# Performance work log

Measured on AMD Instinct MI355X. Metric: run time of the kernel, lower is better.

The kernel has to match this reference:

```python
import jax, jax.numpy as jnp
import numpy as np

B, S, H, F_IN = 256, 128, 512, 1


def _lstm_step(h, c, x, Wih, Whh, b):
    # PyTorch LSTM gate order: i, f, g, o
    gates = x @ Wih.T + h @ Whh.T + b  # (B, 4H)
    i, f, g, o = jnp.split(gates, 4, axis=-1)
    c = jax.nn.sigmoid(f) * c + jax.nn.sigmoid(i) * jnp.tanh(g)
    h = jax.nn.sigmoid(o) * jnp.tanh(c)
    return h, c


def setup_inputs() -> dict:
    key = jax.random.key(0)
    ks = jax.random.split(key, 18)
    p = lambda k, shape: (jax.random.normal(k, shape, dtype=jnp.float32) * 0.05)
    return {
        "input_seq": jax.random.normal(ks[0], (B, S, F_IN), dtype=jnp.float32),
        # encoder: embedding Linear(F_IN -> H) + LSTM(H -> H)
        "We_e": p(ks[1], (H, F_IN)), "be_e": p(ks[2], (H,)),
        "Wih_e": p(ks[3], (4 * H, H)), "Whh_e": p(ks[4], (4 * H, H)), "b_e": p(ks[5], (4 * H,)),
        # decoder: embedding Linear(F_IN -> H) + LSTMCell(H -> H)
        "We_d": p(ks[6], (H, F_IN)), "be_d": p(ks[7], (H,)),
        "Wih_d": p(ks[8], (4 * H, H)), "Whh_d": p(ks[9], (4 * H, H)), "b_d": p(ks[10], (4 * H,)),
        # additive attention: W_1, W_2 (H->H), v (H->1)
        "W1": p(ks[11], (H, H)), "b1": p(ks[12], (H,)),
        "W2": p(ks[13], (H, H)), "b2": p(ks[14], (H,)),
        "v": p(ks[15], (1, H)), "bv": p(ks[16], (1,)),
    }


def reference(input_seq, We_e, be_e, Wih_e, Whh_e, b_e,
              We_d, be_d, Wih_d, Whh_d, b_d,
              W1, b1, W2, b2, v, bv):
    # ---- encoder: embed then LSTM over the sequence ----
    emb = input_seq @ We_e.T + be_e  # (B, S, H)

    def enc_step(carry, x_t):
        h, c = carry
        h, c = _lstm_step(h, c, x_t, Wih_e, Whh_e, b_e)
        return (h, c), h

    h0 = jnp.zeros((B, H), dtype=input_seq.dtype)
    (h, c), enc_h = jax.lax.scan(enc_step, (h0, h0), jnp.swapaxes(emb, 0, 1))
    encoder_output = jnp.swapaxes(enc_h, 0, 1)  # (B, S, H)

    # W_1(encoder_output) is loop-invariant; hoist it (same math as the
    # original, which redundantly recomputes it every step).
    w1enc = encoder_output @ W1.T + b1  # (B, S, H)

    # ---- decoder: per-step LSTMCell + additive attention ----
    def dec_step(carry, _):
        hd, cd, x_in = carry
        e = x_in @ We_d.T + be_d  # (B, H)
        hd, cd = _lstm_step(hd, cd, e, Wih_d, Whh_d, b_d)
        q = hd @ W2.T + b2  # (B, H)
        u = jnp.squeeze(jnp.tanh(w1enc + q[:, None, :]) @ v.T + bv, -1)  # (B, S)
        att = jax.nn.log_softmax(u, axis=1)
        idx = jnp.argmax(att, axis=1)  # pointer (B,)
        # next decoder input = pointed-to input symbol
        x_next = jnp.take_along_axis(input_seq[:, :, 0], idx[:, None], axis=1)  # (B, 1)
        return (hd, cd, x_next), (att, idx)

    x0 = jnp.zeros((B, 1), dtype=input_seq.dtype)
    _, (scores, ptrs) = jax.lax.scan(dec_step, (h, c, x0), None, length=S)
    pointers_scores = jnp.swapaxes(scores, 0, 1)  # (B, S, S) log-probs
    pointers = jnp.swapaxes(ptrs, 0, 1)  # (B, S) int
    return pointers_scores, pointers
```

## Files before the change

kernel.cpp:

```cpp
#include <hip/hip_runtime.h>
#include <hip/hip_fp16.h>

#define Bn 256
#define Sn 128
#define Hn 512
#define G4 2048
#define NBLK 256
#define NTHR 1024
#define HSTR 516

typedef float f4v __attribute__((ext_vector_type(4)));
typedef unsigned u4v __attribute__((ext_vector_type(4)));

__device__ __forceinline__ float sigf(float x){
    float e = expf(-fabsf(x));
    float d = 1.f + e;
    return x >= 0.f ? 1.f/d : e/d;
}

__device__ __forceinline__ float cload(const float* p){
    return __hip_atomic_load((float*)p, __ATOMIC_RELAXED, __HIP_MEMORY_SCOPE_AGENT);
}
__device__ __forceinline__ void cstore(float* p, float v){
    __hip_atomic_store(p, v, __ATOMIC_RELAXED, __HIP_MEMORY_SCOPE_AGENT);
}

__device__ __forceinline__ void gbar(unsigned* cnt, unsigned k){
    __syncthreads();
    if (threadIdx.x == 0) {
        __hip_atomic_fetch_add(cnt, 1u, __ATOMIC_RELAXED, __HIP_MEMORY_SCOPE_AGENT);
        while (__hip_atomic_load(cnt, __ATOMIC_RELAXED, __HIP_MEMORY_SCOPE_AGENT) < 16u*k)
            __builtin_amdgcn_s_sleep(1);
        asm volatile("" ::: "memory");
    }
    __syncthreads();
}
__device__ __forceinline__ void gbar_sys(unsigned* cnt, unsigned k){
    __syncthreads();
    if (threadIdx.x == 0) {
        __hip_atomic_fetch_add(cnt, 1u, __ATOMIC_RELEASE, __HIP_MEMORY_SCOPE_AGENT);
        while (__hip_atomic_load(cnt, __ATOMIC_RELAXED, __HIP_MEMORY_SCOPE_AGENT) < 16u*k)
            __builtin_amdgcn_s_sleep(1);
        (void)__hip_atomic_load(cnt, __ATOMIC_ACQUIRE, __HIP_MEMORY_SCOPE_AGENT);
    }
    __syncthreads();
}

__global__ void precompute_kernel(
    const float* __restrict__ Wih_e, const float* __restrict__ We_e,
    const float* __restrict__ be_e,  const float* __restrict__ b_e,
    const float* __restrict__ Wih_d, const float* __restrict__ We_d,
    const float* __restrict__ be_d,  const float* __restrict__ b_d,
    float* __restrict__ p1, float* __restrict__ p0,
    float* __restrict__ r1, float* __restrict__ r0)
{
    int j = blockIdx.x*blockDim.x + threadIdx.x;
    bool dec = j >= G4;
    int jj = dec ? j - G4 : j;
    const float* Wih = dec ? Wih_d : Wih_e;
    const float* We  = dec ? We_d  : We_e;
    const float* be  = dec ? be_d  : be_e;
    const float* bb  = dec ? b_d   : b_e;
    float s1 = 0.f, s0 = 0.f;
    for (int k = 0; k < Hn; ++k) {
        float w = Wih[jj*Hn + k];
        s1 += w * We[k];
        s0 += w * be[k];
    }
    s0 += bb[jj];
    if (dec) { r1[jj] = s1; r0[jj] = s0; }
    else     { p1[jj] = s1; p0[jj] = s0; }
}

template<bool WEF>
__global__ __launch_bounds__(NTHR, 4) void ptrnet_kernel(
    const float* __restrict__ xseq,
    const float* __restrict__ Whh_e, const float* __restrict__ Whh_d,
    const float* __restrict__ W1, const float* __restrict__ b1,
    const float* __restrict__ W2, const float* __restrict__ b2,
    const float* __restrict__ vv,
    const float* __restrict__ p1, const float* __restrict__ p0,
    const float* __restrict__ r1, const float* __restrict__ r0,
    float* __restrict__ hb0, float* __restrict__ hb1,
    float* __restrict__ cbuf, float* __restrict__ qbuf,
    float* __restrict__ x_in, void* __restrict__ w1enc,
    unsigned* __restrict__ barb,
    float* __restrict__ out_scores, float* __restrict__ out_ptr)
{
    __shared__ float smem[16*HSTR + 512*5 + 16];
    float* hs  = smem;
    float* red = smem + 16*HSTR;
    float* qs  = smem;
    float* vs  = smem + Hn;
    float* us  = smem + 2*Hn;
    float* rr  = smem + 2*Hn + Sn + 8;

    const int blk = blockIdx.x;
    const int tid = threadIdx.x;
    const int bt  = blk >> 4, grp = blk & 15;
    const int b0  = bt << 4;
    const int tb  = tid & 15;
    const int hh  = (tid >> 4) & 31;
    const int ks  = tid >> 9;
    const int hg  = (grp << 5) + hh;
    const int kofs = ks << 8;
    unsigned* gcnt = barb + bt*64;
    unsigned bk = 0;
    float* hprev = hb0;
    float* hnext = hb1;

#define STAGE_H(SRC) do { \
    for (int i_ = tid; i_ < 16*Hn; i_ += NTHR) { \
        int r_ = i_ >> 9, k_ = i_ & (Hn-1); \
        hs[r_*HSTR + k_] = cload((SRC) + (size_t)(b0+r_)*Hn + k_); \
    } __syncthreads(); } while(0)

    for (int t = 0; t <= Sn; ++t) {
        STAGE_H(hprev);
        float a0=0.f,a1=0.f,a2=0.f,a3=0.f,a4=0.f;
        {
            const float* hrow = hs + tb*HSTR + kofs;
            const float* w0 = Whh_e + (size_t)hg*Hn          + kofs;
            const float* w1r= Whh_e + (size_t)(Hn+hg)*Hn     + kofs;
            const float* w2r= Whh_e + (size_t)(2*Hn+hg)*Hn   + kofs;
            const float* w3r= Whh_e + (size_t)(3*Hn+hg)*Hn   + kofs;
            const float* w4r= W1    + (size_t)hg*Hn          + kofs;
            for (int i = 0; i < 256; i += 4) {
                float4 hv = *(const float4*)(hrow + i);
                float4 x0 = *(const float4*)(w0 + i);
                float4 x1 = *(const float4*)(w1r + i);
                float4 x2 = *(const float4*)(w2r + i);
                float4 x3 = *(const float4*)(w3r + i);
                float4 x4 = *(const float4*)(w4r + i);
                a0 += hv.x*x0.x + hv.y*x0.y + hv.z*x0.z + hv.w*x0.w;
                a1 += hv.x*x1.x + hv.y*x1.y + hv.z*x1.z + hv.w*x1.w;
                a2 += hv.x*x2.x + hv.y*x2.y + hv.z*x2.z + hv.w*x2.w;
                a3 += hv.x*x3.x + hv.y*x3.y + hv.z*x3.z + hv.w*x3.w;
                a4 += hv.x*x4.x + hv.y*x4.y + hv.z*x4.z + hv.w*x4.w;
            }
        }
        if (ks) {
            float* rp = red + (size_t)(tid - 512)*5;
            rp[0]=a0; rp[1]=a1; rp[2]=a2; rp[3]=a3; rp[4]=a4;
        }
        __syncthreads();
        if (!ks) {
            const float* rp = red + (size_t)tid*5;
            a0+=rp[0]; a1+=rp[1]; a2+=rp[2]; a3+=rp[3]; a4+=rp[4];
            size_t off = (size_t)(b0+tb)*Hn + hg;
            if (t < Sn) {
                float xv = xseq[(b0+tb)*Sn + t];
                float gi = a0 + xv*p1[hg]      + p0[hg];
                float gf = a1 + xv*p1[Hn+hg]   + p0[Hn+hg];
                float gg = a2 + xv*p1[2*Hn+hg] + p0[2*Hn+hg];
                float go = a3 + xv*p1[3*Hn+hg] + p0[3*Hn+hg];
                float cn = sigf(gf)*cbuf[off] + sigf(gi)*tanhf(gg);
                float hn = sigf(go)*tanhf(cn);
                cbuf[off] = cn;
                cstore(hnext + off, hn);
            }
            if (t > 0) {
                size_t widx = ((size_t)(b0+tb)*Sn + (t-1))*Hn + hg;
                float val = a4 + b1[hg];
                if constexpr (WEF) ((float*)w1enc)[widx] = val;
                else               ((__half*)w1enc)[widx] = __float2half(val);
            }
        }
        ++bk;
        if (t == Sn) gbar_sys(gcnt, bk);
        else         gbar(gcnt, bk);
        if (t < Sn) { float* tp = hprev; hprev = hnext; hnext = tp; }
    }

    for (int t = 0; t < Sn; ++t) {
        STAGE_H(hprev);
        float a0=0.f,a1=0.f,a2=0.f,a3=0.f;
        {
            const float* hrow = hs + tb*HSTR + kofs;
            const float* w0 = Whh_d + (size_t)hg*Hn        + kofs;
            const float* w1r= Whh_d + (size_t)(Hn+hg)*Hn   + kofs;
            const float* w2r= Whh_d + (size_t)(2*Hn+hg)*Hn + kofs;
            const float* w3r= Whh_d + (size_t)(3*Hn+hg)*Hn + kofs;
            for (int i = 0; i < 256; i += 4) {
                float4 hv = *(const float4*)(hrow + i);
                float4 x0 = *(const float4*)(w0 + i);
                float4 x1 = *(const float4*)(w1r + i);
                float4 x2 = *(const float4*)(w2r + i);
                float4 x3 = *(const float4*)(w3r + i);
                a0 += hv.x*x0.x + hv.y*x0.y + hv.z*x0.z + hv.w*x0.w;
                a1 += hv.x*x1.x + hv.y*x1.y + hv.z*x1.z + hv.w*x1.w;
                a2 += hv.x*x2.x + hv.y*x2.y + hv.z*x2.z + hv.w*x2.w;
                a3 += hv.x*x3.x + hv.y*x3.y + hv.z*x3.z + hv.w*x3.w;
            }
        }
        if (ks) {
            float* rp = red + (size_t)(tid - 512)*4;
            rp[0]=a0; rp[1]=a1; rp[2]=a2; rp[3]=a3;
        }
        __syncthreads();
        if (!ks) {
            const float* rp = red + (size_t)tid*4;
            a0+=rp[0]; a1+=rp[1]; a2+=rp[2]; a3+=rp[3];
            size_t off = (size_t)(b0+tb)*Hn + hg;
            float xv = cload(x_in + b0 + tb);
            float gi = a0 + xv*r1[hg]      + r0[hg];
            float gf = a1 + xv*r1[Hn+hg]   + r0[Hn+hg];
            float gg = a2 + xv*r1[2*Hn+hg] + r0[2*Hn+hg];
            float go = a3 + xv*r1[3*Hn+hg] + r0[3*Hn+hg];
            float cn = sigf(gf)*cbuf[off] + sigf(gi)*tanhf(gg);
            float hn = sigf(go)*tanhf(cn);
            cbuf[off] = cn;
            cstore(hnext + off, hn);
        }
        ++bk; gbar(gcnt, bk);
        { float* tp = hprev; hprev = hnext; hnext = tp; }

        STAGE_H(hprev);
        float qa = 0.f;
        {
            const float* hrow = hs + tb*HSTR + kofs;
            const float* wq = W2 + (size_t)hg*Hn + kofs;
            for (int i = 0; i < 256; i += 4) {
                float4 hv = *(const float4*)(hrow + i);
                float4 wv = *(const float4*)(wq + i);
                qa += hv.x*wv.x + hv.y*wv.y + hv.z*wv.z + hv.w*wv.w;
            }
        }
        if (ks) red[tid - 512] = qa;
        __syncthreads();
        if (!ks) cstore(qbuf + (size_t)(b0+tb)*Hn + hg, qa + red[tid] + b2[hg]);
        ++bk; gbar(gcnt, bk);

        if (tid < Hn) qs[tid] = cload(qbuf + (size_t)blk*Hn + tid);
        else          vs[tid - Hn] = vv[tid - Hn];
        __syncthreads();
        const int wv2 = tid >> 6, l = tid & 63;
        const int kb = l << 3;
        float vreg[8], qreg[8];
        #pragma unroll
        for (int j = 0; j < 8; ++j) { vreg[j] = vs[kb+j]; qreg[j] = qs[kb+j]; }
        #pragma unroll
        for (int si = 0; si < 8; ++si) {
            const int s = (wv2 << 3) + si;
            float a = 0.f;
            if constexpr (WEF) {
                const float* wr = (const float*)w1enc + ((size_t)blk*Sn + s)*Hn + kb;
                f4v w0 = __builtin_nontemporal_load((const f4v*)wr);
                f4v w1v = __builtin_nontemporal_load((const f4v*)(wr + 4));
                a += vreg[0]*tanhf(w0[0] + qreg[0]);
                a += vreg[1]*tanhf(w0[1] + qreg[1]);
                a += vreg[2]*tanhf(w0[2] + qreg[2]);
                a += vreg[3]*tanhf(w0[3] + qreg[3]);
                a += vreg[4]*tanhf(w1v[0] + qreg[4]);
                a += vreg[5]*tanhf(w1v[1] + qreg[5]);
                a += vreg[6]*tanhf(w1v[2] + qreg[6]);
                a += vreg[7]*tanhf(w1v[3] + qreg[7]);
            } else {
                const __half* wr = (const __half*)w1enc + ((size_t)blk*Sn + s)*Hn + kb;
                u4v u = __builtin_nontemporal_load((const u4v*)wr);
                unsigned u0=u[0], u1=u[1], u2=u[2], u3=u[3];
                float2 f0 = __half22float2(*(const __half2*)&u0);
                float2 f1 = __half22float2(*(const __half2*)&u1);
                float2 f2 = __half22float2(*(const __half2*)&u2);
                float2 f3 = __half22float2(*(const __half2*)&u3);
                a += vreg[0]*tanhf(f0.x + qreg[0]);
                a += vreg[1]*tanhf(f0.y + qreg[1]);
                a += vreg[2]*tanhf(f1.x + qreg[2]);
                a += vreg[3]*tanhf(f1.y + qreg[3]);
                a += vreg[4]*tanhf(f2.x + qreg[4]);
                a += vreg[5]*tanhf(f2.y + qreg[5]);
                a += vreg[6]*tanhf(f3.x + qreg[6]);
                a += vreg[7]*tanhf(f3.y + qreg[7]);
            }
            a += __shfl_xor(a, 1);  a += __shfl_xor(a, 2);  a += __shfl_xor(a, 4);
            a += __shfl_xor(a, 8);  a += __shfl_xor(a, 16); a += __shfl_xor(a, 32);
            if (l == 0) us[s] = a;
        }
        __syncthreads();
        if (tid < 64) {
            float av = us[tid], c2 = us[tid+64];
            float mv; int mi;
            if (c2 > av) { mv = c2; mi = tid+64; } else { mv = av; mi = tid; }
            #pragma unroll
            for (int off2 = 1; off2 < 64; off2 <<= 1) {
                float ov = __shfl_xor(mv, off2);
                int   oi = __shfl_xor(mi, off2);
                if (ov > mv || (ov == mv && oi < mi)) { mv = ov; mi = oi; }
            }
            float es = expf(av - mv) + expf(c2 - mv);
            #pragma unroll
            for (int off2 = 1; off2 < 64; off2 <<= 1) es += __shfl_xor(es, off2);
            if (tid == 0) {
                rr[0] = mv; rr[1] = logf(es);
                out_ptr[blk*Sn + t] = (float)mi;
                cstore(x_in + blk, xseq[blk*Sn + mi]);
            }
        }
        __syncthreads();
        if (tid < Sn)
            out_scores[((size_t)blk*Sn + t)*Sn + tid] = us[tid] - rr[0] - rr[1];
        if (t < Sn-1) { ++bk; gbar(gcnt, bk); }
    }
#undef STAGE_H
}

extern "C" void kernel_launch(void* const* d_in, const int* in_sizes, int n_in,
                              void* d_out, int out_size, void* d_ws, size_t ws_size,
                              hipStream_t stream)
{
    const float* input_seq = (const float*)d_in[0];
    const float* We_e = (const float*)d_in[1],  *be_e = (const float*)d_in[2];
    const float* Wih_e = (const float*)d_in[3], *Whh_e = (const float*)d_in[4];
    const float* b_e = (const float*)d_in[5];
    const float* We_d = (const float*)d_in[6],  *be_d = (const float*)d_in[7];
    const float* Wih_d = (const float*)d_in[8], *Whh_d = (const float*)d_in[9];
    const float* b_d = (const float*)d_in[10];
    const float* W1 = (const float*)d_in[11], *b1 = (const float*)d_in[12];
    const float* W2 = (const float*)d_in[13], *b2 = (const float*)d_in[14];
    const float* v  = (const float*)d_in[15];

    float* ws = (float*)d_ws;
    size_t o = 0;
    float* hb0  = ws + o; o += Bn*Hn;
    float* hb1  = ws + o; o += Bn*Hn;
    float* cbuf = ws + o; o += Bn*Hn;
    float* qbuf = ws + o; o += Bn*Hn;
    float* p1   = ws + o; o += G4;
    float* p0   = ws + o; o += G4;
    float* r1   = ws + o; o += G4;
    float* r0   = ws + o; o += G4;
    float* x_in = ws + o; o += 256;
    unsigned* barb = (unsigned*)(ws + o); o += 2176;
    void* w1enc = (void*)(ws + o);
    const size_t w1enc_elems = (size_t)Bn*Sn*Hn;
    const size_t need_f32 = (o + w1enc_elems) * sizeof(float);
    const bool wf32 = (ws_size >= need_f32);

    hipMemsetAsync(hb0,  0, Bn*Hn*sizeof(float), stream);
    hipMemsetAsync(cbuf, 0, Bn*Hn*sizeof(float), stream);
    hipMemsetAsync(x_in, 0, (256+2176)*sizeof(float), stream);

    precompute_kernel<<<dim3(16), 256, 0, stream>>>(Wih_e, We_e, be_e, b_e,
                                                    Wih_d, We_d, be_d, b_d,
                                                    p1, p0, r1, r0);

    if (wf32)
        ptrnet_kernel<true ><<<dim3(NBLK), dim3(NTHR), 0, stream>>>(
            input_seq, Whh_e, Whh_d, W1, b1, W2, b2, v,
            p1, p0, r1, r0, hb0, hb1, cbuf, qbuf, x_in, w1enc, barb,
            (float*)d_out, (float*)d_out + (size_t)Bn*Sn*Sn);
    else
        ptrnet_kernel<false><<<dim3(NBLK), dim3(NTHR), 0, stream>>>(
            input_seq, Whh_e, Whh_d, W1, b1, W2, b2, v,
            p1, p0, r1, r0, hb0, hb1, cbuf, qbuf, x_in, w1enc, barb,
            (float*)d_out, (float*)d_out + (size_t)Bn*Sn*Sn);
}
```

Measured before the change: 14.15 ms.

## Fuse decoder q projection into LSTM step via split-K partials, dropping a grid barrier

Each block now computes partial products of W2 against its own 32-wide slice of the freshly computed decoder hidden state and writes them into a per-group partial buffer. The attention phase then sums the 16 partials itself, instead of restaging the whole h, doing a full W2 GEMV and passing another grid barrier. This removes one global barrier and one hidden-state reload per decoder step. The cost is a larger partial buffer in workspace and extra global reads of partials. Hidden-state staging also switches to 64-bit atomic loads, v is hoisted into registers once, and w1enc reads change from nontemporal to normal loads.

```diff
diff --git a/kernel.cpp b/kernel.cpp
--- a/kernel.cpp
+++ b/kernel.cpp
@@ -20,6 +20,12 @@
 
 __device__ __forceinline__ float cload(const float* p){
     return __hip_atomic_load((float*)p, __ATOMIC_RELAXED, __HIP_MEMORY_SCOPE_AGENT);
+}
+__device__ __forceinline__ float2 cload2(const float* p){
+    union { unsigned long long u; float2 f; } cv;
+    cv.u = __hip_atomic_load((const unsigned long long*)p, __ATOMIC_RELAXED,
+                             __HIP_MEMORY_SCOPE_AGENT);
+    return cv.f;
 }
 __device__ __forceinline__ void cstore(float* p, float v){
     __hip_atomic_store(p, v, __ATOMIC_RELAXED, __HIP_MEMORY_SCOPE_AGENT);
@@ -82,18 +88,18 @@
     const float* __restrict__ p1, const float* __restrict__ p0,
     const float* __restrict__ r1, const float* __restrict__ r0,
     float* __restrict__ hb0, float* __restrict__ hb1,
-    float* __restrict__ cbuf, float* __restrict__ qbuf,
+    float* __restrict__ cbuf, float* __restrict__ qpart,
     float* __restrict__ x_in, void* __restrict__ w1enc,
     unsigned* __restrict__ barb,
     float* __restrict__ out_scores, float* __restrict__ out_ptr)
 {
     __shared__ float smem[16*HSTR + 512*5 + 16];
+    __shared__ float hs2[16*36 + 4];
     float* hs  = smem;
     float* red = smem + 16*HSTR;
     float* qs  = smem;
-    float* vs  = smem + Hn;
-    float* us  = smem + 2*Hn;
-    float* rr  = smem + 2*Hn + Sn + 8;
+    float* us  = smem + Hn;
+    float* rr  = smem + Hn + Sn + 8;
 
     const int blk = blockIdx.x;
     const int tid = threadIdx.x;
@@ -109,10 +115,17 @@
     float* hprev = hb0;
     float* hnext = hb1;
 
+    const int l64 = tid & 63;
+    const int kb = l64 << 3;
+    float vreg[8];
+    #pragma unroll
+    for (int j = 0; j < 8; ++j) vreg[j] = vv[kb+j];
+
 #define STAGE_H(SRC) do { \
-    for (int i_ = tid; i_ < 16*Hn; i_ += NTHR) { \
-        int r_ = i_ >> 9, k_ = i_ & (Hn-1); \
-        hs[r_*HSTR + k_] = cload((SRC) + (size_t)(b0+r_)*Hn + k_); \
+    for (int i_ = tid; i_ < 16*256; i_ += NTHR) { \
+        int r_ = i_ >> 8, k2_ = (i_ & 255) << 1; \
+        float2 v2_ = cload2((SRC) + (size_t)(b0+r_)*Hn + k2_); \
+        hs[r_*HSTR + k2_] = v2_.x; hs[r_*HSTR + k2_ + 1] = v2_.y; \
     } __syncthreads(); } while(0)
 
     for (int t = 0; t <= Sn; ++t) {
@@ -211,42 +224,60 @@
             float hn = sigf(go)*tanhf(cn);
             cbuf[off] = cn;
             cstore(hnext + off, hn);
+            hs2[tb*36 + hh] = hn;
+        }
+        __syncthreads();
+        {
+            const int tb2 = tid & 15;
+            const int n0 = (tid >> 4) << 3;
+            const float* h2 = hs2 + tb2*36;
+            float4 h0 = *(const float4*)(h2+0),  h1 = *(const float4*)(h2+4);
+            float4 h2v= *(const float4*)(h2+8),  h3 = *(const float4*)(h2+12);
+            float4 h4 = *(const float4*)(h2+16), h5 = *(const float4*)(h2+20);
+            float4 h6 = *(const float4*)(h2+24), h7 = *(const float4*)(h2+28);
+            float* qp = qpart + ((size_t)(b0+tb2)*Hn + n0)*16 + grp;
+            #pragma unroll
+            for (int n = 0; n < 8; ++n) {
+                const float* wr = W2 + (size_t)(n0+n)*Hn + (grp<<5);
+                float4 w0 = *(const float4*)(wr+0),  w1v= *(const float4*)(wr+4);
+                float4 w2v= *(const float4*)(wr+8),  w3v= *(const float4*)(wr+12);
+                float acc = h0.x*w0.x + h0.y*w0.y + h0.z*w0.z + h0.w*w0.w
+                          + h1.x*w1v.x+ h1.y*w1v.y+ h1.z*w1v.z+ h1.w*w1v.w
+                          + h2v.x*w2v.x+h2v.y*w2v.y+h2v.z*w2v.z+h2v.w*w2v.w
+                          + h3.x*w3v.x+ h3.y*w3v.y+ h3.z*w3v.z+ h3.w*w3v.w;
+                float4 w4 = *(const float4*)(wr+16), w5 = *(const float4*)(wr+20);
+                float4 w6 = *(const float4*)(wr+24), w7 = *(const float4*)(wr+28);
+                acc += h4.x*w4.x + h4.y*w4.y + h4.z*w4.z + h4.w*w4.w
+                     + h5.x*w5.x + h5.y*w5.y + h5.z*w5.z + h5.w*w5.w
+                     + h6.x*w6.x + h6.y*w6.y + h6.z*w6.z + h6.w*w6.w
+                     + h7.x*w7.x + h7.y*w7.y + h7.z*w7.z + h7.w*w7.w;
+                cstore(qp + (size_t)n*16, acc);
+            }
         }
         ++bk; gbar(gcnt, bk);
         { float* tp = hprev; hprev = hnext; hnext = tp; }
 
-        STAGE_H(hprev);
-        float qa = 0.f;
-        {
-            const float* hrow = hs + tb*HSTR + kofs;
-            const float* wq = W2 + (size_t)hg*Hn + kofs;
-            for (int i = 0; i < 256; i += 4) {
-                float4 hv = *(const float4*)(hrow + i);
-                float4 wv = *(const float4*)(wq + i);
-                qa += hv.x*wv.x + hv.y*wv.y + hv.z*wv.z + hv.w*wv.w;
-            }
-        }
-        if (ks) red[tid - 512] = qa;
-        __syncthreads();
-        if (!ks) cstore(qbuf + (size_t)(b0+tb)*Hn + hg, qa + red[tid] + b2[hg]);
-        ++bk; gbar(gcnt, bk);
-
-        if (tid < Hn) qs[tid] = cload(qbuf + (size_t)blk*Hn + tid);
-        else          vs[tid - Hn] = vv[tid - Hn];
-        __syncthreads();
-        const int wv2 = tid >> 6, l = tid & 63;
-        const int kb = l << 3;
-        float vreg[8], qreg[8];
+        const int b = blk;
+        if (tid < Hn) {
+            const float* qp = qpart + ((size_t)b*Hn + tid)*16;
+            float s = b2[tid];
+            #pragma unroll
+            for (int j = 0; j < 16; j += 2) { float2 v2 = cload2(qp + j); s += v2.x + v2.y; }
+            qs[tid] = s;
+        }
+        __syncthreads();
+        const int wv2 = tid >> 6;
+        float qreg[8];
         #pragma unroll
-        for (int j = 0; j < 8; ++j) { vreg[j] = vs[kb+j]; qreg[j] = qs[kb+j]; }
+        for (int j = 0; j < 8; ++j) qreg[j] = qs[kb+j];
         #pragma unroll
         for (int si = 0; si < 8; ++si) {
             const int s = (wv2 << 3) + si;
             float a = 0.f;
             if constexpr (WEF) {
-                const float* wr = (const float*)w1enc + ((size_t)blk*Sn + s)*Hn + kb;
-                f4v w0 = __builtin_nontemporal_load((const f4v*)wr);
-                f4v w1v = __builtin_nontemporal_load((const f4v*)(wr + 4));
+                const float* wr = (const float*)w1enc + ((size_t)b*Sn + s)*Hn + kb;
+                f4v w0 = *(const f4v*)wr;
+                f4v w1v = *(const f4v*)(wr + 4);
                 a += vreg[0]*tanhf(w0[0] + qreg[0]);
                 a += vreg[1]*tanhf(w0[1] + qreg[1]);
                 a += vreg[2]*tanhf(w0[2] + qreg[2]);
@@ -256,8 +287,8 @@
                 a += vreg[6]*tanhf(w1v[2] + qreg[6]);
                 a += vreg[7]*tanhf(w1v[3] + qreg[7]);
             } else {
-                const __half* wr = (const __half*)w1enc + ((size_t)blk*Sn + s)*Hn + kb;
-                u4v u = __builtin_nontemporal_load((const u4v*)wr);
+                const __half* wr = (const __half*)w1enc + ((size_t)b*Sn + s)*Hn + kb;
+                u4v u = *(const u4v*)wr;
                 unsigned u0=u[0], u1=u[1], u2=u[2], u3=u[3];
                 float2 f0 = __half22float2(*(const __half2*)&u0);
                 float2 f1 = __half22float2(*(const __half2*)&u1);
@@ -274,7 +305,7 @@
             }
             a += __shfl_xor(a, 1);  a += __shfl_xor(a, 2);  a += __shfl_xor(a, 4);
             a += __shfl_xor(a, 8);  a += __shfl_xor(a, 16); a += __shfl_xor(a, 32);
-            if (l == 0) us[s] = a;
+            if (l64 == 0) us[s] = a;
         }
         __syncthreads();
         if (tid < 64) {
@@ -292,13 +323,13 @@
             for (int off2 = 1; off2 < 64; off2 <<= 1) es += __shfl_xor(es, off2);
             if (tid == 0) {
                 rr[0] = mv; rr[1] = logf(es);
-                out_ptr[blk*Sn + t] = (float)mi;
-                cstore(x_in + blk, xseq[blk*Sn + mi]);
+                out_ptr[b*Sn + t] = (float)mi;
+                cstore(x_in + b, xseq[b*Sn + mi]);
             }
         }
         __syncthreads();
         if (tid < Sn)
-            out_scores[((size_t)blk*Sn + t)*Sn + tid] = us[tid] - rr[0] - rr[1];
+            out_scores[((size_t)b*Sn + t)*Sn + tid] = us[tid] - rr[0] - rr[1];
         if (t < Sn-1) { ++bk; gbar(gcnt, bk); }
     }
 #undef STAGE_H
@@ -324,13 +355,13 @@
     float* hb0  = ws + o; o += Bn*Hn;
     float* hb1  = ws + o; o += Bn*Hn;
     float* cbuf = ws + o; o += Bn*Hn;
-    float* qbuf = ws + o; o += Bn*Hn;
     float* p1   = ws + o; o += G4;
     float* p0   = ws + o; o += G4;
     float* r1   = ws + o; o += G4;
     float* r0   = ws + o; o += G4;
     float* x_in = ws + o; o += 256;
-    unsigned* barb = (unsigned*)(ws + o); o += 2176;
+    unsigned* barb = (unsigned*)(ws + o); o += 1024;
+    float* qpart = ws + o; o += (size_t)Bn*Hn*16;
     void* w1enc = (void*)(ws + o);
     const size_t w1enc_elems = (size_t)Bn*Sn*Hn;
     const size_t need_f32 = (o + w1enc_elems) * sizeof(float);
@@ -338,7 +369,7 @@
 
     hipMemsetAsync(hb0,  0, Bn*Hn*sizeof(float), stream);
     hipMemsetAsync(cbuf, 0, Bn*Hn*sizeof(float), stream);
-    hipMemsetAsync(x_in, 0, (256+2176)*sizeof(float), stream);
+    hipMemsetAsync(x_in, 0, (256+1024)*sizeof(float), stream);
 
     precompute_kernel<<<dim3(16), 256, 0, stream>>>(Wih_e, We_e, be_e, b_e,
                                                     Wih_d, We_d, be_d, b_d,
@@ -347,11 +378,11 @@
     if (wf32)
         ptrnet_kernel<true ><<<dim3(NBLK), dim3(NTHR), 0, stream>>>(
             input_seq, Whh_e, Whh_d, W1, b1, W2, b2, v,
-            p1, p0, r1, r0, hb0, hb1, cbuf, qbuf, x_in, w1enc, barb,
+            p1, p0, r1, r0, hb0, hb1, cbuf, qpart, x_in, w1enc, barb,
             (float*)d_out, (float*)d_out + (size_t)Bn*Sn*Sn);
     else
         ptrnet_kernel<false><<<dim3(NBLK), dim3(NTHR), 0, stream>>>(
             input_seq, Whh_e, Whh_d, W1, b1, W2, b2, v,
-            p1, p0, r1, r0, hb0, hb1, cbuf, qbuf, x_in, w1enc, barb,
+            p1, p0, r1, r0, hb0, hb1, cbuf, qpart, x_in, w1enc, barb,
             (float*)d_out, (float*)d_out + (size_t)Bn*Sn*Sn);
 }
```

Result: slower. 24.14 ms (+70.6%).
